# Optimization experiments

Hardware: AMD Instinct MI355X
Metric: run time of the kernel (lower is better)

## Reference

```python
import jax, jax.numpy as jnp
import numpy as np

LONG, LAT, T, B, H, NL = 64, 64, 12, 1024, 256, 2
N = LONG * LAT        # 4096 grid nodes
D = 16 * 16           # 256, lin1_size**2


def _build_adj():
    # Faithful reconstruction of GNNLayer's sparse COO adjacency (duplicates sum,
    # as torch sparse matmul does): identity + symmetric 8-neighbor stencil for
    # interior indices i in [lat+1, (long-1)*lat-1). Each undirected edge is
    # inserted twice (once from each endpoint's loop), so interior weights are 2.
    A = np.zeros((N, N), np.float32)
    A[np.arange(N), np.arange(N)] = 1.0
    i = np.arange(LAT + 1, (LONG - 1) * LAT - 1)
    offs = np.array([-1, 1, LAT, -LAT, LAT - 1, LAT + 1, -LAT - 1, -LAT + 1])
    rows = np.repeat(i, 8)
    cols = (i[:, None] + offs).ravel()
    np.add.at(A, (rows, cols), 1.0)
    np.add.at(A, (cols, rows), 1.0)
    return jnp.asarray(A)


def setup_inputs() -> dict:
    key = jax.random.key(0)
    ks = jax.random.split(key, 12)
    s = lambda k, shape, fan: (jax.random.normal(k, shape, jnp.float32) / np.sqrt(fan)).astype(jnp.float32)
    return {
        "x":  jax.random.normal(ks[0], (T, B, LONG, LAT), jnp.float32),
        "h0": jax.random.normal(ks[1], (NL, B, H), jnp.float32),
        "A":  _build_adj(),
        "W_gnn": s(ks[2], (D, N), N), "b_gnn": jnp.zeros((D,), jnp.float32),
        "W_lin": s(ks[3], (D, D), D), "b_lin": jnp.zeros((D,), jnp.float32),
        "Wih0": s(ks[4], (3 * H, D), D), "Whh0": s(ks[5], (3 * H, H), H),
        "bih0": jnp.zeros((3 * H,), jnp.float32), "bhh0": jnp.zeros((3 * H,), jnp.float32),
        "Wih1": s(ks[6], (3 * H, H), H), "Whh1": s(ks[7], (3 * H, H), H),
        "bih1": jnp.zeros((3 * H,), jnp.float32), "bhh1": jnp.zeros((3 * H,), jnp.float32),
        "Wf0": s(ks[8], (16, H), H), "bf0": jnp.zeros((16,), jnp.float32),
        "Wf1": s(ks[9], (16, 16), 16), "bf1": jnp.zeros((16,), jnp.float32),
        "Wf2": s(ks[10], (1, 16), 16), "bf2": jnp.zeros((1,), jnp.float32),
    }


def _gru_layer(xs, h0, Wih, Whh, bih, bhh):
    # xs: [T, B, In]; PyTorch GRU cell equations, input projection hoisted out of scan.
    xW = jnp.einsum('tbd,hd->tbh', xs, Wih) + bih  # [T, B, 3H]
    def step(h, xw):
        hW = h @ Whh.T + bhh
        ri, zi, ni = jnp.split(xw, 3, axis=-1)
        rh, zh, nh = jnp.split(hW, 3, axis=-1)
        r = jax.nn.sigmoid(ri + rh)
        z = jax.nn.sigmoid(zi + zh)
        n = jnp.tanh(ni + r * nh)
        hn = (1.0 - z) * n + z * h
        return hn, hn
    _, hs = jax.lax.scan(step, h0, xW)
    return hs  # [T, B, H]


def reference(x, h0, A, W_gnn, b_gnn, W_lin, b_lin,
              Wih0, Whh0, bih0, bhh0, Wih1, Whh1, bih1, bhh1,
              Wf0, bf0, Wf1, bf1, Wf2, bf2):
    xf = x.reshape(T, B, N)                                   # flatten grid per step
    h1 = jnp.einsum('tbn,mn->tbm', xf, A)                     # (A @ x^T)^T, all steps at once
    t2 = jax.nn.sigmoid(h1 @ W_gnn.T + b_gnn)                 # GNNLayer lin1 + sigmoid
    t4 = jax.nn.sigmoid(t2 @ W_lin.T + b_lin)                 # HailNet lin1 + sigmoid -> [T,B,256]
    hs = _gru_layer(t4, h0[0], Wih0, Whh0, bih0, bhh0)
    hs = _gru_layer(hs, h0[1], Wih1, Whh1, bih1, bhh1)
    out = hs[-1]                                              # last timestep, [B, H]
    out = jax.nn.sigmoid(out @ Wf0.T + bf0)
    out = jax.nn.sigmoid(out @ Wf1.T + bf1)
    out = jax.nn.sigmoid(out @ Wf2.T + bf2)                   # [B, 1]
    return out
```

## Files before the change

### kernel.cpp

```cpp
#include <hip/hip_runtime.h>
#include <hip/hip_bf16.h>

typedef __bf16 bf16;
typedef __bf16 bf16x4 __attribute__((ext_vector_type(4)));
typedef __bf16 bf16x8 __attribute__((ext_vector_type(8)));
typedef float  f32x4  __attribute__((ext_vector_type(4)));

__device__ __forceinline__ float sigf(float x) { return 1.f / (1.f + __expf(-x)); }
__device__ __forceinline__ float tanhf_fast(float x) { return 1.f - 2.f / (1.f + __expf(2.f * x)); }


__global__ __launch_bounds__(256) void k_weff(const float* __restrict__ A,
                                              const float* __restrict__ Wg,
                                              bf16* __restrict__ Weff) {
    int n = blockIdx.x * 256 + threadIdx.x;
    const int offs[9] = {0, -1, 1, 64, -64, 63, 65, -65, -63};
    float w[9];
    int   m[9];
#pragma unroll
    for (int j = 0; j < 9; j++) {
        int mm = n + offs[j];
        bool ok = (mm >= 0 && mm < 4096);
        m[j] = ok ? mm : 0;
        w[j] = ok ? A[(size_t)n * 4096 + mm] : 0.f;
    }
    int d0 = blockIdx.y * 8;
    for (int d = d0; d < d0 + 8; d++) {
        const float* wr = Wg + (size_t)d * 4096;
        float acc = 0.f;
#pragma unroll
        for (int j = 0; j < 9; j++) acc += w[j] * wr[m[j]];
        Weff[(size_t)d * 4096 + n] = (bf16)acc;
    }
}

__device__ __forceinline__ void prep_conv(const float* __restrict__ a,
                                          bf16* __restrict__ o, int blk) {
    int i = blk * 256 + threadIdx.x;
    o[i] = (bf16)a[i];
}

__device__ __forceinline__ void prep_pack(const float* __restrict__ W,
                                          bf16* __restrict__ out, int blk) {
    int fl = blk * 256 + threadIdx.x;
    int lane = fl & 63;
    int kt = (fl >> 6) & 7;
    int c  = (fl >> 9) % 6;
    int wv = (fl >> 9) / 6;
    int l16 = lane & 15, q = lane >> 4;
    int g = c >> 1;
    int wr = g * 256 + wv * 32 + (c & 1) * 16 + l16;
    const float* p = W + (size_t)wr * 256 + kt * 32 + q * 8;
    float4 f0 = *(const float4*)p, f1 = *(const float4*)(p + 4);
    bf16x8 v;
    v[0] = (bf16)f0.x; v[1] = (bf16)f0.y; v[2] = (bf16)f0.z; v[3] = (bf16)f0.w;
    v[4] = (bf16)f1.x; v[5] = (bf16)f1.y; v[6] = (bf16)f1.z; v[7] = (bf16)f1.w;
    *(bf16x8*)(out + (size_t)fl * 8) = v;
}

__global__ __launch_bounds__(256) void k_prep(const float* __restrict__ Wlin, bf16* __restrict__ WlinB,
                                              const float* __restrict__ Wih0, bf16* __restrict__ Wih0B,
                                              const float* __restrict__ Wih1, bf16* __restrict__ Wih1B,
                                              const float* __restrict__ Whh0, bf16* __restrict__ Wpk0,
                                              const float* __restrict__ Whh1, bf16* __restrict__ Wpk1) {
    int b = blockIdx.x;
    if (b < 256)        prep_conv(Wlin, WlinB, b);
    else if (b < 1024)  prep_conv(Wih0, Wih0B, b - 256);
    else if (b < 1792)  prep_conv(Wih1, Wih1B, b - 1024);
    else if (b < 1888)  prep_pack(Whh0, Wpk0, b - 1792);
    else                prep_pack(Whh1, Wpk1, b - 1888);
}

__global__ __launch_bounds__(256) void k_gemm_x(const float* __restrict__ Ap,
                                                const bf16* __restrict__ Bp,
                                                const float* __restrict__ bias,
                                                bf16* __restrict__ Cp) {
    __shared__ bf16 sA[64 * 72];
    __shared__ bf16 sB[64 * 72];
    const int tid = threadIdx.x;
    const int lane = tid & 63, wv = tid >> 6;
    const int l16 = lane & 15, q = lane >> 4;
    const int row0 = blockIdx.x * 64;
    const int col0 = blockIdx.y * 64;
    const int ar = tid >> 2, ak = (tid & 3) * 16;

    f32x4 acc[4] = {};
    float4 pa0, pa1, pa2, pa3;
    bf16x8 pb0, pb1;

    auto loadA = [&](int k0) {
        const float* p = Ap + (size_t)(row0 + ar) * 4096 + k0 + ak;
        pa0 = *(const float4*)p;
        pa1 = *(const float4*)(p + 4);
        pa2 = *(const float4*)(p + 8);
        pa3 = *(const float4*)(p + 12);
    };
    auto loadB = [&](int k0) {
        const bf16* p = Bp + (size_t)(col0 + ar) * 4096 + k0 + ak;
        pb0 = *(const bf16x8*)p;
        pb1 = *(const bf16x8*)(p + 8);
    };
    auto stage = [&]() {
        bf16x8 v0, v1;
        v0[0] = (bf16)pa0.x; v0[1] = (bf16)pa0.y; v0[2] = (bf16)pa0.z; v0[3] = (bf16)pa0.w;
        v0[4] = (bf16)pa1.x; v0[5] = (bf16)pa1.y; v0[6] = (bf16)pa1.z; v0[7] = (bf16)pa1.w;
        v1[0] = (bf16)pa2.x; v1[1] = (bf16)pa2.y; v1[2] = (bf16)pa2.z; v1[3] = (bf16)pa2.w;
        v1[4] = (bf16)pa3.x; v1[5] = (bf16)pa3.y; v1[6] = (bf16)pa3.z; v1[7] = (bf16)pa3.w;
        *(bf16x8*)(sA + ar * 72 + ak) = v0;
        *(bf16x8*)(sA + ar * 72 + ak + 8) = v1;
        *(bf16x8*)(sB + ar * 72 + ak) = pb0;
        *(bf16x8*)(sB + ar * 72 + ak + 8) = pb1;
    };

    loadA(0);
    loadB(0);
    for (int s = 0; s < 64; s++) {
        stage();
        __syncthreads();
        if (s + 1 < 64) { loadA((s + 1) * 64); loadB((s + 1) * 64); }
#pragma unroll
        for (int kk = 0; kk < 2; kk++) {
            bf16x8 a = *(bf16x8*)(sA + (wv * 16 + l16) * 72 + kk * 32 + q * 8);
#pragma unroll
            for (int tn = 0; tn < 4; tn++) {
                bf16x8 b = *(bf16x8*)(sB + (tn * 16 + l16) * 72 + kk * 32 + q * 8);
                acc[tn] = __builtin_amdgcn_mfma_f32_16x16x32_bf16(a, b, acc[tn], 0, 0, 0);
            }
        }
        __syncthreads();
    }

#pragma unroll
    for (int tn = 0; tn < 4; tn++)
#pragma unroll
        for (int r = 0; r < 4; r++) {
            int row = row0 + wv * 16 + q * 4 + r;
            int col = col0 + tn * 16 + l16;
            Cp[(size_t)row * 256 + col] = (bf16)sigf(acc[tn][r] + bias[col]);
        }
}

template <int K, int NTOT, int ACT, bool AF32>
__global__ __launch_bounds__(256) void k_gemm(const void* __restrict__ Ap,
                                              const bf16* __restrict__ Bp,
                                              const float* __restrict__ bias,
                                              void* __restrict__ Cp) {
    __shared__ bf16 sA[64 * 40];
    __shared__ bf16 sB[256 * 40];
    const int tid = threadIdx.x;
    const int lane = tid & 63, wv = tid >> 6;
    const int l16 = lane & 15, q = lane >> 4;
    const int row0 = blockIdx.x * 64;
    const int col0 = blockIdx.y * 256;
    const int ar = tid >> 2, ak = (tid & 3) * 8;

    f32x4 acc[4][4] = {};
    float4 pa0, pa1;
    bf16x8 pab;
    bf16x8 pb[4];

    auto loadA = [&](int k0) {
        if (AF32) {
            const float* p = (const float*)Ap + (size_t)(row0 + ar) * K + k0 + ak;
            pa0 = *(const float4*)p;
            pa1 = *(const float4*)(p + 4);
        } else {
            const bf16* p = (const bf16*)Ap + (size_t)(row0 + ar) * K + k0 + ak;
            pab = *(const bf16x8*)p;
        }
    };
    auto loadB = [&](int k0) {
#pragma unroll
        for (int i = 0; i < 4; i++) {
            int idx = tid + i * 256;
            int r = idx >> 2, kk = (idx & 3) * 8;
            pb[i] = *(const bf16x8*)(Bp + (size_t)(col0 + r) * K + k0 + kk);
        }
    };
    auto stage = [&]() {
        if (AF32) {
            bf16x8 v;
            v[0] = (bf16)pa0.x; v[1] = (bf16)pa0.y; v[2] = (bf16)pa0.z; v[3] = (bf16)pa0.w;
            v[4] = (bf16)pa1.x; v[5] = (bf16)pa1.y; v[6] = (bf16)pa1.z; v[7] = (bf16)pa1.w;
            *(bf16x8*)(sA + ar * 40 + ak) = v;
        } else {
            *(bf16x8*)(sA + ar * 40 + ak) = pab;
        }
#pragma unroll
        for (int i = 0; i < 4; i++) {
            int idx = tid + i * 256;
            int r = idx >> 2, kk = (idx & 3) * 8;
            *(bf16x8*)(sB + r * 40 + kk) = pb[i];
        }
    };

    loadA(0);
    loadB(0);
    const int S = K / 32;
    for (int s = 0; s < S; s++) {
        stage();
        __syncthreads();
        if (s + 1 < S) { loadA((s + 1) * 32); loadB((s + 1) * 32); }
        bf16x8 af[4], bfr[4];
#pragma unroll
        for (int tm = 0; tm < 4; tm++)
            af[tm] = *(bf16x8*)(sA + (tm * 16 + l16) * 40 + q * 8);
#pragma unroll
        for (int tn = 0; tn < 4; tn++)
            bfr[tn] = *(bf16x8*)(sB + (wv * 64 + tn * 16 + l16) * 40 + q * 8);
#pragma unroll
        for (int tm = 0; tm < 4; tm++)
#pragma unroll
            for (int tn = 0; tn < 4; tn++)
                acc[tm][tn] = __builtin_amdgcn_mfma_f32_16x16x32_bf16(
                    af[tm], bfr[tn], acc[tm][tn], 0, 0, 0);
        __syncthreads();
    }

#pragma unroll
    for (int tm = 0; tm < 4; tm++)
#pragma unroll
        for (int tn = 0; tn < 4; tn++)
#pragma unroll
            for (int r = 0; r < 4; r++) {
                int row = row0 + tm * 16 + q * 4 + r;
                int col = col0 + wv * 64 + tn * 16 + l16;
                float v = acc[tm][tn][r] + bias[col];
                if (ACT == 1)
                    ((bf16*)Cp)[(size_t)row * NTOT + col] = (bf16)sigf(v);
                else
                    ((float*)Cp)[(size_t)row * NTOT + col] = v;
            }
}

__global__ __launch_bounds__(512, 2) void k_gru(const float* __restrict__ xw,
                                                const bf16* __restrict__ Wpk,
                                                const float* __restrict__ bhh,
                                                const float* __restrict__ h0,
                                                bf16* __restrict__ hs_out,
                                                float* __restrict__ hfin) {
    __shared__ bf16 hl[16 * 264];
    __shared__ float xwl[16 * 772];
    const int tid = threadIdx.x, lane = tid & 63, wv = tid >> 6;
    const int l16 = lane & 15, q = lane >> 4;
    const int row0 = blockIdx.x * 16;
    const bf16* wb = Wpk + (size_t)wv * 6 * 8 * 64 * 8;

    float bh[6];
#pragma unroll
    for (int c = 0; c < 6; c++) {
        int g = c >> 1;
        bh[c] = bhh[g * 256 + wv * 32 + (c & 1) * 16 + l16];
    }
    float hreg[2][4];
#pragma unroll
    for (int hc = 0; hc < 2; hc++)
#pragma unroll
        for (int r = 0; r < 4; r++) {
            int row = q * 4 + r, col = wv * 32 + hc * 16 + l16;
            float h = h0[(size_t)(row0 + row) * 256 + col];
            hreg[hc][r] = h;
            hl[row * 264 + col] = (bf16)h;
        }
    __syncthreads();

    for (int t = 0; t < 12; t++) {
        {
            const float* gbase = xw + ((size_t)t * 1024 + row0) * 768;
#pragma unroll
            for (int rr = 0; rr < 2; rr++) {
                int row = wv * 2 + rr;
#pragma unroll
                for (int i = 0; i < 3; i++) {
                    const float* gp = gbase + (size_t)row * 768 + i * 256 + lane * 4;
                    float* lp = xwl + row * 772 + i * 256;
                    __builtin_amdgcn_global_load_lds(
                        (const __attribute__((address_space(1))) void*)gp,
                        (__attribute__((address_space(3))) void*)lp,
                        16, 0, 0);
                }
            }
        }
        f32x4 acc[6] = {};
        bf16x8 bc[6], bn[6];
#pragma unroll
        for (int c = 0; c < 6; c++)
            bc[c] = *(const bf16x8*)(wb + ((size_t)(c * 8 + 0) * 64 + lane) * 8);
#pragma unroll
        for (int kt = 0; kt < 8; kt++) {
            bf16x8 a = *(bf16x8*)(hl + l16 * 264 + kt * 32 + q * 8);
            if (kt < 7) {
#pragma unroll
                for (int c = 0; c < 6; c++)
                    bn[c] = *(const bf16x8*)(wb + ((size_t)(c * 8 + kt + 1) * 64 + lane) * 8);
            }
#pragma unroll
            for (int c = 0; c < 6; c++)
                acc[c] = __builtin_amdgcn_mfma_f32_16x16x32_bf16(a, bc[c], acc[c], 0, 0, 0);
#pragma unroll
            for (int c = 0; c < 6; c++) bc[c] = bn[c];
        }
        __syncthreads();
#pragma unroll
        for (int hc = 0; hc < 2; hc++)
#pragma unroll
            for (int r = 0; r < 4; r++) {
                int row = q * 4 + r, col = wv * 32 + hc * 16 + l16;
                const float* xb = xwl + row * 772 + col;
                float rv = sigf(xb[0] + acc[hc][r] + bh[hc]);
                float zv = sigf(xb[256] + acc[2 + hc][r] + bh[2 + hc]);
                float nv = tanhf_fast(xb[512] + rv * (acc[4 + hc][r] + bh[4 + hc]));
                float hn = (1.f - zv) * nv + zv * hreg[hc][r];
                hreg[hc][r] = hn;
                bf16 hb = (bf16)hn;
                hl[row * 264 + col] = hb;
                if (hs_out) hs_out[((size_t)t * 1024 + row0 + row) * 256 + col] = hb;
            }
        __syncthreads();
    }
    if (hfin) {
#pragma unroll
        for (int hc = 0; hc < 2; hc++)
#pragma unroll
            for (int r = 0; r < 4; r++) {
                int row = q * 4 + r, col = wv * 32 + hc * 16 + l16;
                hfin[(size_t)(row0 + row) * 256 + col] = hreg[hc][r];
            }
    }
}

__global__ __launch_bounds__(256) void k_final(const float* __restrict__ h,
                                               const float* __restrict__ Wf0, const float* __restrict__ bf0,
                                               const float* __restrict__ Wf1, const float* __restrict__ bf1,
                                               const float* __restrict__ Wf2, const float* __restrict__ bf2,
                                               float* __restrict__ out) {
    __shared__ float sh[16 * 257];
    __shared__ float sy0[16 * 17];
    __shared__ float sy1[16 * 17];
    int tid = threadIdx.x;
    int r0 = blockIdx.x * 16;
#pragma unroll
    for (int i = 0; i < 16; i++) {
        int idx = tid + i * 256;
        int rr = idx >> 8, cc = idx & 255;
        sh[rr * 257 + cc] = h[(size_t)(r0 + rr) * 256 + cc];
    }
    __syncthreads();
    int rl = tid >> 4, j = tid & 15;
    float acc = bf0[j];
    for (int k = 0; k < 256; k++) acc += sh[rl * 257 + k] * Wf0[j * 256 + k];
    sy0[rl * 17 + j] = sigf(acc);
    __syncthreads();
    float acc1 = bf1[j];
#pragma unroll
    for (int k = 0; k < 16; k++) acc1 += sy0[rl * 17 + k] * Wf1[j * 16 + k];
    sy1[rl * 17 + j] = sigf(acc1);
    __syncthreads();
    if (tid < 16) {
        float a2 = bf2[0];
#pragma unroll
        for (int k = 0; k < 16; k++) a2 += sy1[tid * 17 + k] * Wf2[k];
        out[r0 + tid] = sigf(a2);
    }
}

extern "C" void kernel_launch(void* const* d_in, const int* in_sizes, int n_in,
                              void* d_out, int out_size, void* d_ws, size_t ws_size,
                              hipStream_t stream) {
    const float* x    = (const float*)d_in[0];
    const float* h0   = (const float*)d_in[1];
    const float* A    = (const float*)d_in[2];
    const float* Wgnn = (const float*)d_in[3];
    const float* bgnn = (const float*)d_in[4];
    const float* Wlin = (const float*)d_in[5];
    const float* blin = (const float*)d_in[6];
    const float* Wih0 = (const float*)d_in[7];
    const float* Whh0 = (const float*)d_in[8];
    const float* bih0 = (const float*)d_in[9];
    const float* bhh0 = (const float*)d_in[10];
    const float* Wih1 = (const float*)d_in[11];
    const float* Whh1 = (const float*)d_in[12];
    const float* bih1 = (const float*)d_in[13];
    const float* bhh1 = (const float*)d_in[14];
    const float* Wf0  = (const float*)d_in[15];
    const float* bf0  = (const float*)d_in[16];
    const float* Wf1  = (const float*)d_in[17];
    const float* bf1  = (const float*)d_in[18];
    const float* Wf2  = (const float*)d_in[19];
    const float* bf2  = (const float*)d_in[20];
    float* out = (float*)d_out;

    char* w = (char*)d_ws;
    bf16* Weff  = (bf16*)w;  w += (size_t)256 * 4096 * 2;
    bf16* WlinB = (bf16*)w;  w += (size_t)256 * 256 * 2;
    bf16* Wih0B = (bf16*)w;  w += (size_t)768 * 256 * 2;
    bf16* Wih1B = (bf16*)w;  w += (size_t)768 * 256 * 2;
    bf16* Wpk0  = (bf16*)w;  w += (size_t)768 * 256 * 2;
    bf16* Wpk1  = (bf16*)w;  w += (size_t)768 * 256 * 2;
    bf16* t2    = (bf16*)w;  w += (size_t)12288 * 256 * 2;
    bf16* t4    = (bf16*)w;  w += (size_t)12288 * 256 * 2;
    float* xwb  = (float*)w;
    bf16*  hs   = (bf16*)(w + (size_t)12288 * 768 * 4);
    float* hfin = (float*)(w + (size_t)12288 * 768 * 4 + (size_t)12288 * 256 * 2);
    w += (size_t)4 * 12288 * 256 * 4;
    (void)ws_size;

    k_weff<<<dim3(16, 32), 256, 0, stream>>>(A, Wgnn, Weff);
    k_prep<<<dim3(1984), 256, 0, stream>>>(Wlin, WlinB, Wih0, Wih0B, Wih1, Wih1B,
                                           Whh0, Wpk0, Whh1, Wpk1);

    k_gemm_x<<<dim3(192, 4), 256, 0, stream>>>(x, Weff, bgnn, t2);
    k_gemm<256, 256, 1, false><<<dim3(192, 1), 256, 0, stream>>>(t2, WlinB, blin, t4);
    k_gemm<256, 768, 0, false><<<dim3(192, 3), 256, 0, stream>>>(t4, Wih0B, bih0, xwb);
    k_gru<<<dim3(64), 512, 0, stream>>>(xwb, Wpk0, bhh0, h0, hs, nullptr);
    k_gemm<256, 768, 0, false><<<dim3(192, 3), 256, 0, stream>>>(hs, Wih1B, bih1, xwb);
    k_gru<<<dim3(64), 512, 0, stream>>>(xwb, Wpk1, bhh1, h0 + (size_t)1024 * 256, nullptr, hfin);
    k_final<<<dim3(64), 256, 0, stream>>>(hfin, Wf0, bf0, Wf1, bf1, Wf2, bf2, out);
}
```

Baseline: 554.6 us.

## Double-buffer shared memory and prefetch two stages ahead in k_gemm_x

The x-projection GEMM now keeps two LDS buffers and two sets of prefetch registers. Global loads for tile s+2 are issued while tile s is computed, and the next tile is staged into the other buffer before the barrier. This halves the barriers per K-step and hides more global-load latency. In exchange it doubles shared memory use and raises register pressure, which could lower occupancy.

```diff
diff --git a/kernel.cpp b/kernel.cpp
--- a/kernel.cpp
+++ b/kernel.cpp
@@ -75,8 +75,8 @@
                                                 const bf16* __restrict__ Bp,
                                                 const float* __restrict__ bias,
                                                 bf16* __restrict__ Cp) {
-    __shared__ bf16 sA[64 * 72];
-    __shared__ bf16 sB[64 * 72];
+    __shared__ bf16 sA0[64 * 72], sA1[64 * 72];
+    __shared__ bf16 sB0[64 * 72], sB1[64 * 72];
     const int tid = threadIdx.x;
     const int lane = tid & 63, wv = tid >> 6;
     const int l16 = lane & 15, q = lane >> 4;
@@ -85,50 +85,72 @@
     const int ar = tid >> 2, ak = (tid & 3) * 16;
 
     f32x4 acc[4] = {};
-    float4 pa0, pa1, pa2, pa3;
-    bf16x8 pb0, pb1;
-
-    auto loadA = [&](int k0) {
-        const float* p = Ap + (size_t)(row0 + ar) * 4096 + k0 + ak;
-        pa0 = *(const float4*)p;
-        pa1 = *(const float4*)(p + 4);
-        pa2 = *(const float4*)(p + 8);
-        pa3 = *(const float4*)(p + 12);
-    };
-    auto loadB = [&](int k0) {
-        const bf16* p = Bp + (size_t)(col0 + ar) * 4096 + k0 + ak;
-        pb0 = *(const bf16x8*)p;
-        pb1 = *(const bf16x8*)(p + 8);
-    };
-    auto stage = [&]() {
-        bf16x8 v0, v1;
-        v0[0] = (bf16)pa0.x; v0[1] = (bf16)pa0.y; v0[2] = (bf16)pa0.z; v0[3] = (bf16)pa0.w;
-        v0[4] = (bf16)pa1.x; v0[5] = (bf16)pa1.y; v0[6] = (bf16)pa1.z; v0[7] = (bf16)pa1.w;
-        v1[0] = (bf16)pa2.x; v1[1] = (bf16)pa2.y; v1[2] = (bf16)pa2.z; v1[3] = (bf16)pa2.w;
-        v1[4] = (bf16)pa3.x; v1[5] = (bf16)pa3.y; v1[6] = (bf16)pa3.z; v1[7] = (bf16)pa3.w;
-        *(bf16x8*)(sA + ar * 72 + ak) = v0;
-        *(bf16x8*)(sA + ar * 72 + ak + 8) = v1;
-        *(bf16x8*)(sB + ar * 72 + ak) = pb0;
-        *(bf16x8*)(sB + ar * 72 + ak + 8) = pb1;
-    };
-
-    loadA(0);
-    loadB(0);
-    for (int s = 0; s < 64; s++) {
-        stage();
-        __syncthreads();
-        if (s + 1 < 64) { loadA((s + 1) * 64); loadB((s + 1) * 64); }
-#pragma unroll
-        for (int kk = 0; kk < 2; kk++) {
-            bf16x8 a = *(bf16x8*)(sA + (wv * 16 + l16) * 72 + kk * 32 + q * 8);
-#pragma unroll
-            for (int tn = 0; tn < 4; tn++) {
-                bf16x8 b = *(bf16x8*)(sB + (tn * 16 + l16) * 72 + kk * 32 + q * 8);
-                acc[tn] = __builtin_amdgcn_mfma_f32_16x16x32_bf16(a, b, acc[tn], 0, 0, 0);
-            }
-        }
-        __syncthreads();
-    }
+    float4 paA0, paA1, paA2, paA3, paB0, paB1, paB2, paB3;
+    bf16x8 pbA0, pbA1, pbB0, pbB1;
+
+    const float* Abase = Ap + (size_t)(row0 + ar) * 4096 + ak;
+    const bf16*  Bbase = Bp + (size_t)(col0 + ar) * 4096 + ak;
+
+#define LOAD_A(k0, r0_, r1_, r2_, r3_)                  \
+    { const float* p = Abase + (k0);                    \
+      r0_ = *(const float4*)p;                          \
+      r1_ = *(const float4*)(p + 4);                    \
+      r2_ = *(const float4*)(p + 8);                    \
+      r3_ = *(const float4*)(p + 12); }
+#define LOAD_B(k0, r0_, r1_)                            \
+    { const bf16* p = Bbase + (k0);                     \
+      r0_ = *(const bf16x8*)p;                          \
+      r1_ = *(const bf16x8*)(p + 8); }
+#define STAGE(dA, dB, a0_, a1_, a2_, a3_, b0_, b1_)     \
+    { bf16x8 v0, v1;                                     \
+      v0[0] = (bf16)a0_.x; v0[1] = (bf16)a0_.y; v0[2] = (bf16)a0_.z; v0[3] = (bf16)a0_.w; \
+      v0[4] = (bf16)a1_.x; v0[5] = (bf16)a1_.y; v0[6] = (bf16)a1_.z; v0[7] = (bf16)a1_.w; \
+      v1[0] = (bf16)a2_.x; v1[1] = (bf16)a2_.y; v1[2] = (bf16)a2_.z; v1[3] = (bf16)a2_.w; \
+      v1[4] = (bf16)a3_.x; v1[5] = (bf16)a3_.y; v1[6] = (bf16)a3_.z; v1[7] = (bf16)a3_.w; \
+      *(bf16x8*)(dA + ar * 72 + ak) = v0;               \
+      *(bf16x8*)(dA + ar * 72 + ak + 8) = v1;           \
+      *(bf16x8*)(dB + ar * 72 + ak) = b0_;              \
+      *(bf16x8*)(dB + ar * 72 + ak + 8) = b1_; }
+#define COMPUTE(cA, cB)                                  \
+    _Pragma("unroll")                                    \
+    for (int kk = 0; kk < 2; kk++) {                     \
+        bf16x8 a = *(bf16x8*)(cA + (wv * 16 + l16) * 72 + kk * 32 + q * 8); \
+        _Pragma("unroll")                                \
+        for (int tn = 0; tn < 4; tn++) {                 \
+            bf16x8 b = *(bf16x8*)(cB + (tn * 16 + l16) * 72 + kk * 32 + q * 8); \
+            acc[tn] = __builtin_amdgcn_mfma_f32_16x16x32_bf16(a, b, acc[tn], 0, 0, 0); \
+        }                                                \
+    }
+
+    LOAD_A(0, paA0, paA1, paA2, paA3);
+    LOAD_B(0, pbA0, pbA1);
+    STAGE(sA0, sB0, paA0, paA1, paA2, paA3, pbA0, pbA1);
+    LOAD_A(64, paA0, paA1, paA2, paA3);
+    LOAD_B(64, pbA0, pbA1);
+    __syncthreads();
+
+    for (int s = 0; s < 64; s += 2) {
+        if (s + 2 < 64) {
+            LOAD_A((s + 2) * 64, paB0, paB1, paB2, paB3);
+            LOAD_B((s + 2) * 64, pbB0, pbB1);
+        }
+        COMPUTE(sA0, sB0);
+        STAGE(sA1, sB1, paA0, paA1, paA2, paA3, pbA0, pbA1);
+        __syncthreads();
+        if (s + 3 < 64) {
+            LOAD_A((s + 3) * 64, paA0, paA1, paA2, paA3);
+            LOAD_B((s + 3) * 64, pbA0, pbA1);
+        }
+        COMPUTE(sA1, sB1);
+        if (s + 2 < 64) {
+            STAGE(sA0, sB0, paB0, paB1, paB2, paB3, pbB0, pbB1);
+        }
+        __syncthreads();
+    }
+#undef LOAD_A
+#undef LOAD_B
+#undef STAGE
+#undef COMPUTE
 
 #pragma unroll
     for (int tn = 0; tn < 4; tn++)
```

New measurement: 562.1 us. Within noise of the previous version (+1.4%).
